# Performance work log

Hardware: AMD Instinct MI355X
Metric: run time of the kernel (lower is better)

## Reference

```python
import jax, jax.numpy as jnp
import numpy as np

# ---- SLAYER neuron / simulation params (netParams) ----
THETA = 10.0      # spike threshold
TAU_SR = 10.0     # PSP (SRM alpha) time constant
TAU_REF = 1.0     # refractory time constant
TAU_RHO = 1.0     # surrogate-gradient width factor (pdfTimeConstant = tauRho*theta)
SCALE_RHO = 1.0
TS = 1.0
T_SAMPLE = 300

def _alpha_kernel(tau, mult, eps=0.01):
    # replicates slayer._calculateAlphaKernel: truncated alpha kernel
    vals = []
    for t in np.arange(0.0, T_SAMPLE, TS):
        v = mult * t / tau * np.exp(1.0 - t / tau)
        if abs(v) < eps and t > tau:
            break
        vals.append(v)
    return jnp.asarray(np.array(vals, np.float32))

SRM = _alpha_kernel(TAU_SR, 1.0)              # ~77-tap causal PSP filter
REF = _alpha_kernel(TAU_REF, -2.0 * THETA)    # short refractory kernel (REF[0]=0)


def psp(x):
    """Causal FIR filter along last (time) axis: y[t] = sum_s x[t-s]*SRM[s]."""
    K = SRM.shape[0]
    sh = x.shape
    T = sh[-1]
    xr = x.reshape(-1, 1, T)                 # (M, 1, T)
    w = SRM[::-1].reshape(1, 1, K)           # reversed for cross-correlation
    y = jax.lax.conv_general_dilated(xr, w, (1,), [(K - 1, 0)])
    return y.reshape(sh)


def _spike_scan(u):
    """LIF/SRM spike generation with refractory feedback (slayerCuda.getSpikes).
    Returns (spikes, effective membrane potential incl. refractory)."""
    sh = u.shape
    T = sh[-1]
    uf = u.reshape(-1, T).T                  # (T, M)
    K = REF.shape[0]
    M = uf.shape[1]

    def step(buf, ut):
        # buf[k] = refractory contribution to membrane at time t+k from past spikes
        ueff = ut + buf[0]
        s = (ueff >= THETA).astype(ut.dtype)  # spike value 1/Ts with Ts=1
        buf = buf + s[None, :] * REF[:, None]  # REF[0]=0, so current step unaffected
        buf = jnp.concatenate([buf[1:], jnp.zeros((1, M), ut.dtype)], axis=0)
        return buf, (s, ueff)

    _, (S, U) = jax.lax.scan(step, jnp.zeros((K, M), u.dtype), uf)
    return S.T.reshape(sh), U.T.reshape(sh)


@jax.custom_vjp
def spike(u):
    return _spike_scan(u)[0]

def _spike_fwd(u):
    s, ueff = _spike_scan(u)
    return s, ueff

def _spike_bwd(ueff, g):
    # SLAYER surrogate gradient: pdfScale/pdfTimeConstant * exp(-|u - theta|/pdfTimeConstant)
    tc = TAU_RHO * THETA
    return (g * (SCALE_RHO / tc) * jnp.exp(-jnp.abs(ueff - THETA) / tc),)

spike.defvjp(_spike_fwd, _spike_bwd)


def conv3(x, w, pad):
    # spatial conv per time step: x (N,C,H,W,T), w (O,I,kh,kw,1)
    dn = jax.lax.conv_dimension_numbers(x.shape, w.shape, ('NCHWT', 'OIHWT', 'NCHWT'))
    return jax.lax.conv_general_dilated(
        x, w, (1, 1, 1), [(pad, pad), (pad, pad), (0, 0)], dimension_numbers=dn)


def pool2(x):
    # slayer pool: 2x2 sum-pool per channel, fixed weight 1.1*theta/(k*k)
    N, C, H, W, T = x.shape
    return x.reshape(N, C, H // 2, 2, W // 2, 2, T).sum(axis=(3, 5)) * (1.1 * THETA / 4.0)


def dense(x, w):
    # slayer dense((8,8,64),10): full-spatial conv == linear over (C,H,W) per time step
    y = jnp.einsum('nchwt,ochw->not', x, w)
    return y[:, :, None, None, :]             # (N,10,1,1,T)


def _forward(x, w1, w2, w3, wfc):
    s1 = spike(conv3(psp(x), w1, 1))          # (N,16,32,32,T)
    s2 = spike(pool2(psp(s1)))                # (N,16,16,16,T)
    s3 = spike(conv3(psp(s2), w2, 1))         # (N,32,16,16,T)
    s4 = spike(pool2(psp(s3)))                # (N,32,8,8,T)
    s5 = spike(conv3(psp(s4), w3, 1))         # (N,64,8,8,T)
    return spike(dense(psp(s5), wfc))         # (N,10,1,1,T)


def setup_inputs() -> dict:
    key = jax.random.key(0)
    k = jax.random.split(key, 5)
    x = (jax.random.uniform(k[0], (8, 2, 34, 34, 300)) < 0.05).astype(jnp.float32)
    w1 = jax.random.normal(k[1], (16, 2, 5, 5, 1), jnp.float32) * 0.5
    w2 = jax.random.normal(k[2], (32, 16, 3, 3, 1), jnp.float32) * 0.2
    w3 = jax.random.normal(k[3], (64, 32, 3, 3, 1), jnp.float32) * 0.15
    wfc = jax.random.normal(k[4], (10, 64, 8, 8), jnp.float32) * 0.05
    return {"spikeInput": x, "w1": w1, "w2": w2, "w3": w3, "wfc": wfc}


def reference(spikeInput, w1, w2, w3, wfc):
    return _forward(spikeInput, w1, w2, w3, wfc)
```

## Files before the change

kernel.cpp:

```cpp
#include <hip/hip_runtime.h>
#include <cmath>

#define THETA 10.0f

__device__ __forceinline__ void init_srm(float* srm) {
    int tid = threadIdx.x;
    if (tid < 77) {
        double td = (double)tid;
        srm[tid] = (float)(td / 10.0 * exp(1.0 - td / 10.0));
    }
    __syncthreads();
}

__global__ void transpose_kernel(const float* __restrict__ in, float* __restrict__ out,
                                 int M, int T) {
    __shared__ float tile[32][33];
    int mBase = blockIdx.x * 32;
    int tBase = blockIdx.y * 32;
    int tx = threadIdx.x, ty = threadIdx.y;
    for (int i = ty; i < 32; i += 8) {
        int m = mBase + i, t = tBase + tx;
        if (m < M && t < T) tile[i][tx] = in[(size_t)m * T + t];
    }
    __syncthreads();
    for (int i = ty; i < 32; i += 8) {
        int t = tBase + i, m = mBase + tx;
        if (t < T && m < M) out[(size_t)t * M + m] = tile[tx][i];
    }
}

template <int TT>
__global__ void psp_kernel(const float* __restrict__ in, float* __restrict__ out,
                           int M) {
    __shared__ float srm_s[77];
    init_srm(srm_s);
    int tb = blockIdx.y * TT;
    int m = blockIdx.x * blockDim.x + threadIdx.x;
    if (m >= M) return;
    float c[77];
#pragma unroll
    for (int s = 0; s < 77; ++s) c[s] = srm_s[s];
    float acc[TT];
#pragma unroll
    for (int j = 0; j < TT; ++j) acc[j] = 0.f;
#pragma unroll
    for (int k = TT - 1; k >= 0; --k) {
        float v = in[(size_t)(tb + k) * M + m];
#pragma unroll
        for (int j = k; j < TT; ++j) acc[j] = fmaf(v, c[j - k], acc[j]);
    }
#pragma unroll
    for (int s0 = 1; s0 <= 77 - TT; ++s0) {
        int u = tb - s0;
        if (u >= 0) {
            float v = in[(size_t)u * M + m];
#pragma unroll
            for (int j = 0; j < TT; ++j) acc[j] = fmaf(v, c[s0 + j], acc[j]);
        }
    }
#pragma unroll
    for (int k = 78 - TT; k <= 76; ++k) {
        int u = tb - k;
        if (u >= 0) {
            float v = in[(size_t)u * M + m];
#pragma unroll
            for (int j = 0; j <= 76 - k; ++j) acc[j] = fmaf(v, c[k + j], acc[j]);
        }
    }
#pragma unroll
    for (int j = 0; j < TT; ++j) out[(size_t)(tb + j) * M + m] = acc[j];
}

template <int TT>
__global__ void psp_u8_kernel(const unsigned char* __restrict__ in,
                              float* __restrict__ out, int M) {
    __shared__ float srm_s[77];
    init_srm(srm_s);
    int tb = blockIdx.y * TT;
    int m = blockIdx.x * blockDim.x + threadIdx.x;
    if (m >= M) return;
    float c[77];
#pragma unroll
    for (int s = 0; s < 77; ++s) c[s] = srm_s[s];
    float acc[TT];
#pragma unroll
    for (int j = 0; j < TT; ++j) acc[j] = 0.f;
#pragma unroll
    for (int k = TT - 1; k >= 0; --k) {
        float v = (float)in[(size_t)(tb + k) * M + m];
#pragma unroll
        for (int j = k; j < TT; ++j) acc[j] = fmaf(v, c[j - k], acc[j]);
    }
#pragma unroll
    for (int s0 = 1; s0 <= 77 - TT; ++s0) {
        int u = tb - s0;
        if (u >= 0) {
            float v = (float)in[(size_t)u * M + m];
#pragma unroll
            for (int j = 0; j < TT; ++j) acc[j] = fmaf(v, c[s0 + j], acc[j]);
        }
    }
#pragma unroll
    for (int k = 78 - TT; k <= 76; ++k) {
        int u = tb - k;
        if (u >= 0) {
            float v = (float)in[(size_t)u * M + m];
#pragma unroll
            for (int j = 0; j <= 76 - k; ++j) acc[j] = fmaf(v, c[k + j], acc[j]);
        }
    }
#pragma unroll
    for (int j = 0; j < TT; ++j) out[(size_t)(tb + j) * M + m] = acc[j];
}

template <int TT>
__global__ void psppool_u8_kernel(const unsigned char* __restrict__ in,
                                  float* __restrict__ out,
                                  int NC, int Hin, int Win) {
    __shared__ float srm_s[77];
    init_srm(srm_s);
    int Ho = Hin >> 1, Wo = Win >> 1;
    int Mout = NC * Ho * Wo;
    int Min = NC * Hin * Win;
    int tb = blockIdx.y * TT;
    int mo = blockIdx.x * blockDim.x + threadIdx.x;
    if (mo >= Mout) return;
    int X = mo % Wo;
    int Y = (mo / Wo) % Ho;
    int nc = mo / (Wo * Ho);
    int base = nc * Hin * Win + (2 * Y) * Win + 2 * X;
    float c[77];
#pragma unroll
    for (int s = 0; s < 77; ++s) c[s] = srm_s[s];
    float acc[TT];
#pragma unroll
    for (int j = 0; j < TT; ++j) acc[j] = 0.f;
#pragma unroll
    for (int k = TT - 1; k >= 0; --k) {
        const unsigned char* p = in + (size_t)(tb + k) * Min + base;
        uchar2 a0 = *reinterpret_cast<const uchar2*>(p);
        uchar2 a1 = *reinterpret_cast<const uchar2*>(p + Win);
        float v = (float)((int)a0.x + (int)a0.y + (int)a1.x + (int)a1.y);
#pragma unroll
        for (int j = k; j < TT; ++j) acc[j] = fmaf(c[j - k], v, acc[j]);
    }
#pragma unroll
    for (int s0 = 1; s0 <= 77 - TT; ++s0) {
        int u = tb - s0;
        if (u >= 0) {
            const unsigned char* p = in + (size_t)u * Min + base;
            uchar2 a0 = *reinterpret_cast<const uchar2*>(p);
            uchar2 a1 = *reinterpret_cast<const uchar2*>(p + Win);
            float v = (float)((int)a0.x + (int)a0.y + (int)a1.x + (int)a1.y);
#pragma unroll
            for (int j = 0; j < TT; ++j) acc[j] = fmaf(c[s0 + j], v, acc[j]);
        }
    }
#pragma unroll
    for (int k = 78 - TT; k <= 76; ++k) {
        int u = tb - k;
        if (u >= 0) {
            const unsigned char* p = in + (size_t)u * Min + base;
            uchar2 a0 = *reinterpret_cast<const uchar2*>(p);
            uchar2 a1 = *reinterpret_cast<const uchar2*>(p + Win);
            float v = (float)((int)a0.x + (int)a0.y + (int)a1.x + (int)a1.y);
#pragma unroll
            for (int j = 0; j <= 76 - k; ++j) acc[j] = fmaf(c[k + j], v, acc[j]);
        }
    }
#pragma unroll
    for (int j = 0; j < TT; ++j)
        out[(size_t)(tb + j) * Mout + mo] = acc[j] * 2.75f;
}

__global__ __launch_bounds__(256) void conv1_v4(const float* __restrict__ in,
                                                const float* __restrict__ w,
                                                float* __restrict__ out) {
    __shared__ float s_in[2592];
    __shared__ float s_w[800];
    int n = blockIdx.x, t = blockIdx.y, tid = threadIdx.x;
    const float* src = in + ((size_t)t * 8 + n) * 2312;
    for (int idx = tid; idx < 2592; idx += 256) {
        int ch = idx / 1296, rem = idx % 1296;
        int r = rem / 36, col = rem % 36;
        float v = 0.f;
        if (r >= 1 && r <= 34 && col >= 1 && col <= 34)
            v = src[ch * 1156 + (r - 1) * 34 + (col - 1)];
        s_in[idx] = v;
    }
    for (int idx = tid; idx < 800; idx += 256) {
        int tap = idx >> 4, o = idx & 15;
        s_w[tap * 16 + o] = w[o * 50 + tap];
    }
    __syncthreads();
    int x = tid & 31, y0 = tid >> 5;
    float acc[4][16];
#pragma unroll
    for (int q = 0; q < 4; ++q)
#pragma unroll
        for (int o = 0; o < 16; ++o) acc[q][o] = 0.f;
#pragma unroll
    for (int i = 0; i < 2; ++i) {
#pragma unroll
        for (int ky = 0; ky < 5; ++ky) {
#pragma unroll
            for (int kx = 0; kx < 5; ++kx) {
                int tap = i * 25 + ky * 5 + kx;
                float v[4];
#pragma unroll
                for (int q = 0; q < 4; ++q)
                    v[q] = s_in[i * 1296 + (y0 + 8 * q + ky) * 36 + (x + kx)];
                const float4* wp = (const float4*)&s_w[tap * 16];
#pragma unroll
                for (int oq = 0; oq < 4; ++oq) {
                    float4 w4 = wp[oq];
#pragma unroll
                    for (int q = 0; q < 4; ++q) {
                        acc[q][oq * 4 + 0] = fmaf(v[q], w4.x, acc[q][oq * 4 + 0]);
                        acc[q][oq * 4 + 1] = fmaf(v[q], w4.y, acc[q][oq * 4 + 1]);
                        acc[q][oq * 4 + 2] = fmaf(v[q], w4.z, acc[q][oq * 4 + 2]);
                        acc[q][oq * 4 + 3] = fmaf(v[q], w4.w, acc[q][oq * 4 + 3]);
                    }
                }
            }
        }
    }
    float* dst = out + ((size_t)t * 8 + n) * 16384;
#pragma unroll
    for (int q = 0; q < 4; ++q) {
        int y = y0 + 8 * q;
#pragma unroll
        for (int o = 0; o < 16; ++o) dst[o * 1024 + y * 32 + x] = acc[q][o];
    }
}

__global__ __launch_bounds__(256) void conv2_v3(const float* __restrict__ in,
                                                const float* __restrict__ w,
                                                float* __restrict__ out) {
    __shared__ float s_in[5184];
    int n = blockIdx.x, t = blockIdx.y, ob = blockIdx.z * 16;
    int tid = threadIdx.x;
    const float* src = in + ((size_t)t * 8 + n) * 4096;
    for (int idx = tid; idx < 5184; idx += 256) {
        int c = idx / 324, rem = idx % 324;
        int r = rem / 18, col = rem % 18;
        float v = 0.f;
        if (r >= 1 && r <= 16 && col >= 1 && col <= 16)
            v = src[c * 256 + (r - 1) * 16 + (col - 1)];
        s_in[idx] = v;
    }
    __syncthreads();
    int x = tid & 15, y = tid >> 4;
    float acc[16];
#pragma unroll
    for (int o = 0; o < 16; ++o) acc[o] = 0.f;
    for (int i = 0; i < 16; ++i) {
        const float* base = &s_in[i * 324 + y * 18 + x];
        float vv[9];
#pragma unroll
        for (int ky = 0; ky < 3; ++ky)
#pragma unroll
            for (int kx = 0; kx < 3; ++kx) vv[ky * 3 + kx] = base[ky * 18 + kx];
#pragma unroll
        for (int tap = 0; tap < 9; ++tap) {
            float v = vv[tap];
            const float* wp = w + (size_t)ob * 144 + i * 9 + tap;
#pragma unroll
            for (int o = 0; o < 16; ++o)
                acc[o] = fmaf(v, wp[o * 144], acc[o]);
        }
    }
    float* dst = out + (((size_t)t * 8 + n) * 32 + ob) * 256;
#pragma unroll
    for (int o = 0; o < 16; ++o) dst[o * 256 + tid] = acc[o];
}

__global__ __launch_bounds__(256) void conv3_v3(const float* __restrict__ in,
                                                const float* __restrict__ w,
                                                float* __restrict__ out) {
    __shared__ float s_in[8192];
    int n0 = blockIdx.x * 4, t = blockIdx.y, ob = blockIdx.z * 16;
    int tid = threadIdx.x;
    const float* src = in + ((size_t)t * 16384 + n0 * 2048);
    for (int i = tid; i < 8192; i += 256) s_in[i] = src[i];
    __syncthreads();
    int ln = tid >> 6;
    int pos = tid & 63;
    int y = pos >> 3, x = pos & 7;
    bool mask[9];
    int off[9];
#pragma unroll
    for (int ky = 0; ky < 3; ++ky) {
        int iy = y + ky - 1;
        bool ry = (unsigned)iy < 8u;
#pragma unroll
        for (int kx = 0; kx < 3; ++kx) {
            int ix = x + kx - 1;
            bool ok = ry && ((unsigned)ix < 8u);
            mask[ky * 3 + kx] = ok;
            off[ky * 3 + kx] = ok ? (iy * 8 + ix) : 0;
        }
    }
    const float* base = &s_in[ln * 2048];
    float acc[16];
#pragma unroll
    for (int o = 0; o < 16; ++o) acc[o] = 0.f;
    for (int i = 0; i < 32; ++i) {
        const float* ip = base + i * 64;
        float vv[9];
#pragma unroll
        for (int tap = 0; tap < 9; ++tap)
            vv[tap] = mask[tap] ? ip[off[tap]] : 0.f;
#pragma unroll
        for (int tap = 0; tap < 9; ++tap) {
            float v = vv[tap];
            const float* wp = w + (size_t)ob * 288 + i * 9 + tap;
#pragma unroll
            for (int o = 0; o < 16; ++o)
                acc[o] = fmaf(v, wp[o * 288], acc[o]);
        }
    }
    float* dst = out + (((size_t)t * 8 + n0 + ln) * 64 + ob) * 64;
#pragma unroll
    for (int o = 0; o < 16; ++o) dst[o * 64 + pos] = acc[o];
}

template <int CH>
__global__ void spike_u8_kernel(const float* __restrict__ u,
                                unsigned char* __restrict__ sp, int M, int T) {
    int m = blockIdx.x * blockDim.x + threadIdx.x;
    if (m >= M) return;
    float ref[11];
#pragma unroll
    for (int k = 0; k < 11; ++k)
        ref[k] = (float)(-20.0 * (double)k * exp(1.0 - (double)k));
    float r[11];
#pragma unroll
    for (int k = 0; k < 11; ++k) r[k] = 0.f;
    float a[CH], b[CH];
#pragma unroll
    for (int j = 0; j < CH; ++j) a[j] = u[(size_t)j * M + m];
    int NC = T / CH;
    for (int c = 0; c < NC; ++c) {
        if (c + 1 < NC) {
#pragma unroll
            for (int j = 0; j < CH; ++j)
                b[j] = u[(size_t)((c + 1) * CH + j) * M + m];
        }
#pragma unroll
        for (int j = 0; j < CH; ++j) {
            float ue = a[j] + r[0];
            float s = (ue >= THETA) ? 1.0f : 0.0f;
            sp[(size_t)(c * CH + j) * M + m] = (unsigned char)(ue >= THETA);
#pragma unroll
            for (int k = 0; k < 10; ++k) r[k] = fmaf(s, ref[k + 1], r[k + 1]);
        }
#pragma unroll
        for (int j = 0; j < CH; ++j) a[j] = b[j];
    }
}

__global__ void dense_kernel(const float* __restrict__ p, const float* __restrict__ wfc,
                             float* __restrict__ out) {
    int n = blockIdx.x;
    int t = blockIdx.y;
    int tid = threadIdx.x;
    const float* row = p + ((size_t)t * 8 + n) * 4096;
    float acc[10];
#pragma unroll
    for (int o = 0; o < 10; ++o) acc[o] = 0.f;
    for (int j = tid; j < 4096; j += 256) {
        float v = row[j];
#pragma unroll
        for (int o = 0; o < 10; ++o) acc[o] = fmaf(v, wfc[o * 4096 + j], acc[o]);
    }
    __shared__ float red[4][10];
#pragma unroll
    for (int o = 0; o < 10; ++o) {
        float a = acc[o];
        for (int off = 32; off > 0; off >>= 1) a += __shfl_down(a, off, 64);
        acc[o] = a;
    }
    int wave = tid >> 6, lane = tid & 63;
    if (lane == 0) {
#pragma unroll
        for (int o = 0; o < 10; ++o) red[wave][o] = acc[o];
    }
    __syncthreads();
    if (tid < 10) {
        float a = (red[0][tid] + red[1][tid]) + (red[2][tid] + red[3][tid]);
        out[((size_t)t * 8 + n) * 10 + tid] = a;
    }
}

template <int CH>
__global__ void spike_out_kernel(const float* __restrict__ u, float* __restrict__ out,
                                 int M, int T) {
    int m = blockIdx.x * blockDim.x + threadIdx.x;
    if (m >= M) return;
    float ref[11];
#pragma unroll
    for (int k = 0; k < 11; ++k)
        ref[k] = (float)(-20.0 * (double)k * exp(1.0 - (double)k));
    float r[11];
#pragma unroll
    for (int k = 0; k < 11; ++k) r[k] = 0.f;
    float a[CH], b[CH];
#pragma unroll
    for (int j = 0; j < CH; ++j) a[j] = u[(size_t)j * M + m];
    int NC = T / CH;
    for (int c = 0; c < NC; ++c) {
        if (c + 1 < NC) {
#pragma unroll
            for (int j = 0; j < CH; ++j)
                b[j] = u[(size_t)((c + 1) * CH + j) * M + m];
        }
#pragma unroll
        for (int j = 0; j < CH; ++j) {
            float ue = a[j] + r[0];
            float s = (ue >= THETA) ? 1.0f : 0.0f;
            out[(size_t)m * T + c * CH + j] = s;
#pragma unroll
            for (int k = 0; k < 10; ++k) r[k] = fmaf(s, ref[k + 1], r[k + 1]);
        }
#pragma unroll
        for (int j = 0; j < CH; ++j) a[j] = b[j];
    }
}

extern "C" void kernel_launch(void* const* d_in, const int* in_sizes, int n_in,
                              void* d_out, int out_size, void* d_ws, size_t ws_size,
                              hipStream_t stream) {
    const float* x   = (const float*)d_in[0];
    const float* w1  = (const float*)d_in[1];
    const float* w2  = (const float*)d_in[2];
    const float* w3  = (const float*)d_in[3];
    const float* wfc = (const float*)d_in[4];
    float* outp = (float*)d_out;

    float* slotB = (float*)d_ws;
    float* slotA = slotB + 39321600;
    unsigned char* s1_u8 = (unsigned char*)(slotA + 9830400);
    unsigned char* sB_u8 = (unsigned char*)(slotB + 9830400);
    unsigned char* s5_u8 = (unsigned char*)slotA;
    const int T = 300;
    dim3 blk(256);
    dim3 blk64(64);
    constexpr int TT = 20;
    constexpr int CH = 10;

    transpose_kernel<<<dim3(578, 10), dim3(32, 8), 0, stream>>>(x, slotB, 18496, T);
    psp_kernel<TT><<<dim3(73, 15), blk, 0, stream>>>(slotB, slotA, 18496);
    conv1_v4<<<dim3(8, T), blk, 0, stream>>>(slotA, w1, slotB);
    spike_u8_kernel<CH><<<dim3(2048), blk64, 0, stream>>>(slotB, s1_u8, 131072, T);
    psppool_u8_kernel<TT><<<dim3(128, 15), blk, 0, stream>>>(s1_u8, slotA, 8 * 16, 32, 32);
    spike_u8_kernel<CH><<<dim3(512), blk64, 0, stream>>>(slotA, sB_u8, 32768, T);
    psp_u8_kernel<TT><<<dim3(128, 15), blk, 0, stream>>>(sB_u8, slotB, 32768);
    conv2_v3<<<dim3(8, T, 2), blk, 0, stream>>>(slotB, w2, slotA);
    spike_u8_kernel<CH><<<dim3(1024), blk64, 0, stream>>>(slotA, sB_u8, 65536, T);
    psppool_u8_kernel<TT><<<dim3(64, 15), blk, 0, stream>>>(sB_u8, slotB, 8 * 32, 16, 16);
    spike_u8_kernel<CH><<<dim3(256), blk64, 0, stream>>>(slotB, sB_u8, 16384, T);
    psp_u8_kernel<TT><<<dim3(64, 15), blk, 0, stream>>>(sB_u8, slotA, 16384);
    conv3_v3<<<dim3(2, T, 4), blk, 0, stream>>>(slotA, w3, slotB);
    spike_u8_kernel<CH><<<dim3(512), blk64, 0, stream>>>(slotB, s5_u8, 32768, T);
    psp_u8_kernel<TT><<<dim3(128, 15), blk, 0, stream>>>(s5_u8, slotB, 32768);
    float* u6 = slotA + 16000000;
    dense_kernel<<<dim3(8, T), blk, 0, stream>>>(slotB, wfc, u6);
    spike_out_kernel<CH><<<dim3(2), dim3(64), 0, stream>>>(u6, outp, 80, T);
}
```

Before: 830.2 us.

## Register-block conv2 and conv3 over two timesteps and 32 output channels

Conv2 and conv3 now process two timesteps per block and 32 output channels per thread, so each weight load is reused for two FMAs and input tiles are staged once for more outputs. Conv2 drops the output-channel grid split and computes all 32 channels per block. Conv3 moves to 128-thread blocks covering two batch items with a 32-channel split. This cuts global weight loads and launch count per output, but doubles accumulator registers (64 per thread), which may reduce occupancy or cause spills.

```diff
diff --git a/kernel.cpp b/kernel.cpp
--- a/kernel.cpp
+++ b/kernel.cpp
@@ -234,55 +234,77 @@
     }
 }
 
-__global__ __launch_bounds__(256) void conv2_v3(const float* __restrict__ in,
+__global__ __launch_bounds__(256) void conv2_v5(const float* __restrict__ in,
                                                 const float* __restrict__ w,
                                                 float* __restrict__ out) {
-    __shared__ float s_in[5184];
-    int n = blockIdx.x, t = blockIdx.y, ob = blockIdx.z * 16;
+    __shared__ float s_in[2][5184];
+    int n = blockIdx.x;
+    int tp = blockIdx.y;
     int tid = threadIdx.x;
-    const float* src = in + ((size_t)t * 8 + n) * 4096;
-    for (int idx = tid; idx < 5184; idx += 256) {
-        int c = idx / 324, rem = idx % 324;
-        int r = rem / 18, col = rem % 18;
-        float v = 0.f;
-        if (r >= 1 && r <= 16 && col >= 1 && col <= 16)
-            v = src[c * 256 + (r - 1) * 16 + (col - 1)];
-        s_in[idx] = v;
+    float* flat = (float*)s_in;
+    for (int idx = tid; idx < 10368; idx += 256) flat[idx] = 0.f;
+    __syncthreads();
+#pragma unroll
+    for (int tt = 0; tt < 2; ++tt) {
+        const float* src = in + ((size_t)(2 * tp + tt) * 8 + n) * 4096;
+        for (int idx = tid; idx < 4096; idx += 256) {
+            int c = idx >> 8, r = (idx >> 4) & 15, col = idx & 15;
+            s_in[tt][c * 324 + (r + 1) * 18 + (col + 1)] = src[idx];
+        }
     }
     __syncthreads();
     int x = tid & 15, y = tid >> 4;
-    float acc[16];
-#pragma unroll
-    for (int o = 0; o < 16; ++o) acc[o] = 0.f;
+    float acc[2][32];
+#pragma unroll
+    for (int tt = 0; tt < 2; ++tt)
+#pragma unroll
+        for (int o = 0; o < 32; ++o) acc[tt][o] = 0.f;
     for (int i = 0; i < 16; ++i) {
-        const float* base = &s_in[i * 324 + y * 18 + x];
-        float vv[9];
+        const float* b0 = &s_in[0][i * 324 + y * 18 + x];
+        const float* b1 = &s_in[1][i * 324 + y * 18 + x];
+        float v0[9], v1[9];
 #pragma unroll
         for (int ky = 0; ky < 3; ++ky)
 #pragma unroll
-            for (int kx = 0; kx < 3; ++kx) vv[ky * 3 + kx] = base[ky * 18 + kx];
+            for (int kx = 0; kx < 3; ++kx) {
+                v0[ky * 3 + kx] = b0[ky * 18 + kx];
+                v1[ky * 3 + kx] = b1[ky * 18 + kx];
+            }
 #pragma unroll
         for (int tap = 0; tap < 9; ++tap) {
-            float v = vv[tap];
-            const float* wp = w + (size_t)ob * 144 + i * 9 + tap;
-#pragma unroll
-            for (int o = 0; o < 16; ++o)
-                acc[o] = fmaf(v, wp[o * 144], acc[o]);
-        }
-    }
-    float* dst = out + (((size_t)t * 8 + n) * 32 + ob) * 256;
-#pragma unroll
-    for (int o = 0; o < 16; ++o) dst[o * 256 + tid] = acc[o];
-}
-
-__global__ __launch_bounds__(256) void conv3_v3(const float* __restrict__ in,
+            float a0 = v0[tap], a1 = v1[tap];
+            const float* wp = w + i * 9 + tap;
+#pragma unroll
+            for (int o = 0; o < 32; ++o) {
+                float ww = wp[o * 144];
+                acc[0][o] = fmaf(a0, ww, acc[0][o]);
+                acc[1][o] = fmaf(a1, ww, acc[1][o]);
+            }
+        }
+    }
+#pragma unroll
+    for (int tt = 0; tt < 2; ++tt) {
+        float* dst = out + ((size_t)(2 * tp + tt) * 8 + n) * 8192;
+#pragma unroll
+        for (int o = 0; o < 32; ++o) dst[o * 256 + tid] = acc[tt][o];
+    }
+}
+
+__global__ __launch_bounds__(128) void conv3_v5(const float* __restrict__ in,
                                                 const float* __restrict__ w,
                                                 float* __restrict__ out) {
-    __shared__ float s_in[8192];
-    int n0 = blockIdx.x * 4, t = blockIdx.y, ob = blockIdx.z * 16;
+    __shared__ float s_in[2][2][2048];
+    int n0 = blockIdx.x * 2;
+    int tp = blockIdx.y;
+    int ob = blockIdx.z * 32;
     int tid = threadIdx.x;
-    const float* src = in + ((size_t)t * 16384 + n0 * 2048);
-    for (int i = tid; i < 8192; i += 256) s_in[i] = src[i];
+    float* flat = (float*)s_in;
+#pragma unroll
+    for (int tt = 0; tt < 2; ++tt) {
+        const float* src = in + ((size_t)(2 * tp + tt) * 8 + n0) * 2048;
+        for (int idx = tid; idx < 4096; idx += 128)
+            flat[tt * 4096 + idx] = src[idx];
+    }
     __syncthreads();
     int ln = tid >> 6;
     int pos = tid & 63;
@@ -301,28 +323,38 @@
             off[ky * 3 + kx] = ok ? (iy * 8 + ix) : 0;
         }
     }
-    const float* base = &s_in[ln * 2048];
-    float acc[16];
-#pragma unroll
-    for (int o = 0; o < 16; ++o) acc[o] = 0.f;
+    float acc[2][32];
+#pragma unroll
+    for (int tt = 0; tt < 2; ++tt)
+#pragma unroll
+        for (int o = 0; o < 32; ++o) acc[tt][o] = 0.f;
     for (int i = 0; i < 32; ++i) {
-        const float* ip = base + i * 64;
-        float vv[9];
-#pragma unroll
-        for (int tap = 0; tap < 9; ++tap)
-            vv[tap] = mask[tap] ? ip[off[tap]] : 0.f;
+        const float* ip0 = &s_in[0][ln][i * 64];
+        const float* ip1 = &s_in[1][ln][i * 64];
+        float v0[9], v1[9];
 #pragma unroll
         for (int tap = 0; tap < 9; ++tap) {
-            float v = vv[tap];
+            v0[tap] = mask[tap] ? ip0[off[tap]] : 0.f;
+            v1[tap] = mask[tap] ? ip1[off[tap]] : 0.f;
+        }
+#pragma unroll
+        for (int tap = 0; tap < 9; ++tap) {
+            float a0 = v0[tap], a1 = v1[tap];
             const float* wp = w + (size_t)ob * 288 + i * 9 + tap;
 #pragma unroll
-            for (int o = 0; o < 16; ++o)
-                acc[o] = fmaf(v, wp[o * 288], acc[o]);
-        }
-    }
-    float* dst = out + (((size_t)t * 8 + n0 + ln) * 64 + ob) * 64;
-#pragma unroll
-    for (int o = 0; o < 16; ++o) dst[o * 64 + pos] = acc[o];
+            for (int o = 0; o < 32; ++o) {
+                float ww = wp[o * 288];
+                acc[0][o] = fmaf(a0, ww, acc[0][o]);
+                acc[1][o] = fmaf(a1, ww, acc[1][o]);
+            }
+        }
+    }
+#pragma unroll
+    for (int tt = 0; tt < 2; ++tt) {
+        float* dst = out + (((size_t)(2 * tp + tt) * 8 + n0 + ln) * 64 + ob) * 64;
+#pragma unroll
+        for (int o = 0; o < 32; ++o) dst[o * 64 + pos] = acc[tt][o];
+    }
 }
 
 template <int CH>
@@ -456,12 +488,12 @@
     psppool_u8_kernel<TT><<<dim3(128, 15), blk, 0, stream>>>(s1_u8, slotA, 8 * 16, 32, 32);
     spike_u8_kernel<CH><<<dim3(512), blk64, 0, stream>>>(slotA, sB_u8, 32768, T);
     psp_u8_kernel<TT><<<dim3(128, 15), blk, 0, stream>>>(sB_u8, slotB, 32768);
-    conv2_v3<<<dim3(8, T, 2), blk, 0, stream>>>(slotB, w2, slotA);
+    conv2_v5<<<dim3(8, 150), blk, 0, stream>>>(slotB, w2, slotA);
     spike_u8_kernel<CH><<<dim3(1024), blk64, 0, stream>>>(slotA, sB_u8, 65536, T);
     psppool_u8_kernel<TT><<<dim3(64, 15), blk, 0, stream>>>(sB_u8, slotB, 8 * 32, 16, 16);
     spike_u8_kernel<CH><<<dim3(256), blk64, 0, stream>>>(slotB, sB_u8, 16384, T);
     psp_u8_kernel<TT><<<dim3(64, 15), blk, 0, stream>>>(sB_u8, slotA, 16384);
-    conv3_v3<<<dim3(2, T, 4), blk, 0, stream>>>(slotA, w3, slotB);
+    conv3_v5<<<dim3(4, 150, 2), dim3(128), 0, stream>>>(slotA, w3, slotB);
     spike_u8_kernel<CH><<<dim3(512), blk64, 0, stream>>>(slotB, s5_u8, 32768, T);
     psp_u8_kernel<TT><<<dim3(128, 15), blk, 0, stream>>>(s5_u8, slotB, 32768);
     float* u6 = slotA + 16000000;
```

Result: slower. 931.4 us (+12.2%).
